# Kernel tuning notes

Measured on AMD Instinct MI355X. Metric: run time of the kernel, lower is better.

## Reference

```python
import jax, jax.numpy as jnp
import numpy as np

D_MODEL = 1024
NUM_HEADS = 16
HEAD_DIM = D_MODEL // NUM_HEADS
B, S, L_CACHE = 2, 1024, 1024


def setup_inputs() -> dict:
    key = jax.random.key(0)
    ks = jax.random.split(key, 12)
    sc = 1.0 / np.sqrt(D_MODEL)
    return {
        "x": jax.random.normal(ks[0], (B, S, D_MODEL), jnp.float32),
        "cache_k": jax.random.normal(ks[1], (B, NUM_HEADS, L_CACHE, HEAD_DIM), jnp.float32),
        "cache_v": jax.random.normal(ks[2], (B, NUM_HEADS, L_CACHE, HEAD_DIM), jnp.float32),
        "Wq": jax.random.normal(ks[3], (D_MODEL, D_MODEL), jnp.float32) * sc,
        "bq": jax.random.normal(ks[4], (D_MODEL,), jnp.float32) * 0.01,
        "Wk": jax.random.normal(ks[5], (D_MODEL, D_MODEL), jnp.float32) * sc,
        "bk": jax.random.normal(ks[6], (D_MODEL,), jnp.float32) * 0.01,
        "Wv": jax.random.normal(ks[7], (D_MODEL, D_MODEL), jnp.float32) * sc,
        "bv": jax.random.normal(ks[8], (D_MODEL,), jnp.float32) * 0.01,
        "Wo": jax.random.normal(ks[9], (D_MODEL, D_MODEL), jnp.float32) * sc,
        "bo": jax.random.normal(ks[10], (D_MODEL,), jnp.float32) * 0.01,
    }


def reference(x, cache_k, cache_v, Wq, bq, Wk, bk, Wv, bv, Wo, bo):
    b, s, d = x.shape
    h, hd = NUM_HEADS, HEAD_DIM
    # torch Linear: y = x @ W^T + b
    def proj(W, bias):
        y = jnp.einsum('bsd,ed->bse', x, W) + bias
        return y.reshape(b, s, h, hd).transpose(0, 2, 1, 3)  # [B,H,S,hd]
    Q = proj(Wq, bq)
    K = jnp.concatenate([cache_k, proj(Wk, bk)], axis=2)  # [B,H,T,hd]
    V = jnp.concatenate([cache_v, proj(Wv, bv)], axis=2)
    T = K.shape[2]
    scores = jnp.einsum('bhqd,bhkd->bhqk', Q, K) / jnp.sqrt(jnp.float32(hd))
    # causal mask with cache offset: query i sees keys j <= i + (T - s)
    offset = T - s
    q_idx = jnp.arange(s)[:, None]
    k_idx = jnp.arange(T)[None, :]
    mask = k_idx > (q_idx + offset)  # [S,T], True = masked
    scores = jnp.where(mask[None, None], -jnp.inf, scores)
    attn = jax.nn.softmax(scores, axis=-1)
    out = jnp.einsum('bhqk,bhkd->bhqd', attn, V)
    out = out.transpose(0, 2, 1, 3).reshape(b, s, d)
    return jnp.einsum('bsd,ed->bse', out, Wo) + bo
```

## Files before the change

kernel.cpp:

```cpp
#include <hip/hip_runtime.h>
#include <hip/hip_bf16.h>
#include <stdint.h>

typedef __bf16 bf16;
typedef __bf16 bf16x4 __attribute__((ext_vector_type(4)));
typedef __bf16 bf16x8 __attribute__((ext_vector_type(8)));
typedef float  f32x4  __attribute__((ext_vector_type(4)));

#define DEV __device__ __forceinline__

#define BB 2
#define HH 16
#define SS 1024
#define DD 1024
#define HD 64
#define LC 1024
#define TT 2048
#define OFFS 1024

DEV f32x4 mfma16(bf16x8 a, bf16x8 b, f32x4 c) {
    return __builtin_amdgcn_mfma_f32_16x16x32_bf16(a, b, c, 0, 0, 0);
}

DEV void async_load16(const bf16* g, bf16* lds) {
    auto gp = reinterpret_cast<const __attribute__((address_space(1))) void*>(
        reinterpret_cast<uintptr_t>(g));
    auto lp = reinterpret_cast<__attribute__((address_space(3))) void*>(
        reinterpret_cast<uintptr_t>(lds));
    __builtin_amdgcn_global_load_lds(gp, lp, 16, 0, 0);
}

__global__ __launch_bounds__(256) void cvt_all(
    const float* __restrict__ x,  bf16* __restrict__ xb,
    const float* __restrict__ w0, const float* __restrict__ w1,
    const float* __restrict__ w2, const float* __restrict__ w3,
    bf16* __restrict__ d0, bf16* __restrict__ d1,
    bf16* __restrict__ d2, bf16* __restrict__ d3,
    const float* __restrict__ ck, bf16* __restrict__ Kf,
    const float* __restrict__ cv, bf16* __restrict__ Vt) {
    __shared__ float tile[64][65];
    const int bid = blockIdx.x;
    const int tid = threadIdx.x;
    if (bid < 8192) {
        const float* s;
        bf16* d;
        int i;
        if (bid < 2048) {
            s = x; d = xb; i = bid * 256 + tid;
        } else if (bid < 6144) {
            int which = (bid - 2048) >> 10;
            s = which == 0 ? w0 : which == 1 ? w1 : which == 2 ? w2 : w3;
            d = which == 0 ? d0 : which == 1 ? d1 : which == 2 ? d2 : d3;
            i = ((bid - 2048) & 1023) * 256 + tid;
        } else {
            int ii = (bid - 6144) * 256 + tid;
            int bh  = ii >> 14;
            int rem = ii & 16383;
            float4 v = ((const float4*)ck)[ii];
            bf16x4 o;
            o[0] = (bf16)v.x; o[1] = (bf16)v.y; o[2] = (bf16)v.z; o[3] = (bf16)v.w;
            ((bf16x4*)(Kf + (size_t)bh * TT * HD))[rem] = o;
            return;
        }
        float4 v = ((const float4*)s)[i];
        bf16x4 o;
        o[0] = (bf16)v.x; o[1] = (bf16)v.y; o[2] = (bf16)v.z; o[3] = (bf16)v.w;
        ((bf16x4*)d)[i] = o;
    } else {
        int rem = bid - 8192;
        int bh = rem >> 4;
        int t0 = (rem & 15) * 64;
        int c4 = (tid & 15) * 4;
        int rr = tid >> 4;
        const float* src = cv + ((size_t)bh * LC + t0) * HD;
#pragma unroll
        for (int p = 0; p < 4; ++p) {
            int t = rr + p * 16;
            float4 v = *(const float4*)(src + (size_t)t * HD + c4);
            tile[c4 + 0][t] = v.x; tile[c4 + 1][t] = v.y;
            tile[c4 + 2][t] = v.z; tile[c4 + 3][t] = v.w;
        }
        __syncthreads();
        bf16* dst = Vt + (size_t)bh * HD * TT + t0;
#pragma unroll
        for (int p = 0; p < 4; ++p) {
            int d = rr + p * 16;
            int tc = (tid & 15) * 4;
            bf16x4 o;
            o[0] = (bf16)tile[d][tc + 0]; o[1] = (bf16)tile[d][tc + 1];
            o[2] = (bf16)tile[d][tc + 2]; o[3] = (bf16)tile[d][tc + 3];
            *(bf16x4*)(dst + (size_t)d * TT + tc) = o;
        }
    }
}

__global__ __launch_bounds__(256) void gemm_nt(
    const bf16* __restrict__ A, const bf16* __restrict__ W,
    const float* __restrict__ bq, const float* __restrict__ bk,
    const float* __restrict__ bv, const float* __restrict__ bo,
    bf16* __restrict__ Qb, bf16* __restrict__ Kf, bf16* __restrict__ Vt,
    float* __restrict__ Out, int is_oproj) {
    const int tid  = threadIdx.x;
    const int wv   = tid >> 6;
    const int lane = tid & 63;
    const int l16  = lane & 15;
    const int quad = lane >> 4;
    const int m0 = blockIdx.y * 64;
    const int n0 = blockIdx.x * 128;
    const int mode = is_oproj ? 3 : (n0 >> 10);
    const float* bias = (mode == 0) ? bq : (mode == 1) ? bk : (mode == 2) ? bv : bo;

    __shared__ __align__(16) bf16 As[2][64 * 64];
    __shared__ __align__(16) bf16 Bs[2][128 * 64];

    f32x4 acc[4][2];
#pragma unroll
    for (int i = 0; i < 4; ++i)
#pragma unroll
        for (int j = 0; j < 2; ++j) {
            f32x4 z = {0.f, 0.f, 0.f, 0.f};
            acc[i][j] = z;
        }

    auto stage = [&](int k0, int b) {
#pragma unroll
        for (int k = 0; k < 2; ++k) {
            int seg = k * 256 + tid;
            int row = seg >> 3;
            int c   = (seg & 7) ^ (row & 7);
            async_load16(A + (size_t)(m0 + row) * 1024 + k0 + c * 8, &As[b][seg * 8]);
        }
#pragma unroll
        for (int k = 0; k < 4; ++k) {
            int seg = k * 256 + tid;
            int row = seg >> 3;
            int c   = (seg & 7) ^ (row & 7);
            async_load16(W + (size_t)(n0 + row) * 1024 + k0 + c * 8, &Bs[b][seg * 8]);
        }
    };

    stage(0, 0);

    for (int it = 0; it < 16; ++it) {
        __syncthreads();
        const bf16* Ab = &As[it & 1][0];
        const bf16* Bb = &Bs[it & 1][0];
        if (it + 1 < 16) stage((it + 1) * 64, (it + 1) & 1);

#pragma unroll
        for (int kk = 0; kk < 2; ++kk) {
            bf16x8 af[4], bfr[2];
#pragma unroll
            for (int i = 0; i < 4; ++i) {
                int row = i * 16 + l16;
                int slot = (kk * 4 + quad) ^ (row & 7);
                af[i] = *(const bf16x8*)(Ab + (row * 8 + slot) * 8);
            }
#pragma unroll
            for (int j = 0; j < 2; ++j) {
                int row = wv * 32 + j * 16 + l16;
                int slot = (kk * 4 + quad) ^ (row & 7);
                bfr[j] = *(const bf16x8*)(Bb + (row * 8 + slot) * 8);
            }
#pragma unroll
            for (int i = 0; i < 4; ++i)
#pragma unroll
                for (int j = 0; j < 2; ++j)
                    acc[i][j] = mfma16(af[i], bfr[j], acc[i][j]);
        }
    }

#pragma unroll
    for (int i = 0; i < 4; ++i) {
#pragma unroll
        for (int j = 0; j < 2; ++j) {
            int n = n0 + wv * 32 + j * 16 + l16;
            float bval = bias[n & 1023];
#pragma unroll
            for (int r = 0; r < 4; ++r) {
                int m = m0 + i * 16 + quad * 4 + r;
                float v = acc[i][j][r] + bval;
                if (mode == 3) {
                    Out[(size_t)m * 1024 + n] = v;
                } else {
                    int b = m >> 10, s = m & 1023;
                    int h = (n & 1023) >> 6, d = n & 63;
                    int bh = b * HH + h;
                    if (mode == 0)
                        Qb[((size_t)bh * SS + s) * HD + d] = (bf16)v;
                    else if (mode == 1)
                        Kf[((size_t)bh * TT + LC + s) * HD + d] = (bf16)v;
                    else
                        Vt[((size_t)bh * HD + d) * TT + LC + s] = (bf16)v;
                }
            }
        }
    }
}

__global__ __launch_bounds__(256) void attn(const bf16* __restrict__ Qb,
                                            const bf16* __restrict__ Kf,
                                            const bf16* __restrict__ Vt,
                                            bf16* __restrict__ Ob) {
    const int i = blockIdx.x;
    const int bh = i & 31;
    const int qblk = (i < 256) ? (15 - (i >> 5)) : ((i >> 5) - 8);
    const int tid  = threadIdx.x;
    const int wv   = tid >> 6;
    const int lane = tid & 63;
    const int l16  = lane & 15;
    const int quad = lane >> 4;
    const int qb   = qblk * 64;
    const int qw   = qb + wv * 16;

    const bf16* Qp = Qb + ((size_t)bh * SS + qw) * HD;
    const bf16* Kp = Kf + (size_t)bh * TT * HD;
    const bf16* Vp = Vt + (size_t)bh * HD * TT;

    __shared__ __align__(16) bf16 Ks[2][64 * 64];
    __shared__ __align__(16) bf16 Vs[2][64 * 64];

    bf16x8 qf0 = *(const bf16x8*)(Qp + l16 * HD + quad * 8);
    bf16x8 qf1 = *(const bf16x8*)(Qp + l16 * HD + 32 + quad * 8);

    float lsum = 0.f;
    f32x4 o[4];
#pragma unroll
    for (int dt = 0; dt < 4; ++dt) {
        f32x4 z = {0.f, 0.f, 0.f, 0.f};
        o[dt] = z;
    }

    const int niters = qblk + 17;

    auto stage = [&](int tile, int b) {
        const int t0 = tile * 64;
#pragma unroll
        for (int j = 0; j < 2; ++j) {
            int seg = (j * 4 + wv) * 64 + lane;
            int row = seg >> 3;
            int gc  = (seg & 7) ^ (row & 7);
            async_load16(Kp + (size_t)(t0 + row) * HD + gc * 8, &Ks[b][seg * 8]);
            async_load16(Vp + (size_t)row * TT + t0 + gc * 8, &Vs[b][seg * 8]);
        }
    };

    stage(0, 0);

    const float C1 = 0.18033688f;
    const float C2 = -11.5415603f;

    for (int it = 0; it < niters; ++it) {
        __syncthreads();
        const bf16* Kb = &Ks[it & 1][0];
        const bf16* Vb = &Vs[it & 1][0];
        if (it + 1 < niters) stage(it + 1, (it + 1) & 1);

        const int t0 = it * 64;
        const bool full = (t0 + 63 <= qw + OFFS);

        f32x4 s[4];
#pragma unroll
        for (int kt = 0; kt < 4; ++kt) {
            int row = kt * 16 + l16;
            int swz = row & 7;
            bf16x8 ka = *(const bf16x8*)(Kb + (row * 8 + (quad ^ swz)) * 8);
            bf16x8 kb = *(const bf16x8*)(Kb + (row * 8 + ((4 + quad) ^ swz)) * 8);
            f32x4 z = {0.f, 0.f, 0.f, 0.f};
            z = mfma16(ka, qf0, z);
            z = mfma16(kb, qf1, z);
            s[kt] = z;
        }

        f32x4 p[4];
        if (full) {
#pragma unroll
            for (int kt = 0; kt < 4; ++kt)
#pragma unroll
                for (int r = 0; r < 4; ++r)
                    p[kt][r] = __builtin_amdgcn_exp2f(fmaf(s[kt][r], C1, C2));
        } else {
            const int qlim = qw + l16 + OFFS - t0;
#pragma unroll
            for (int kt = 0; kt < 4; ++kt)
#pragma unroll
                for (int r = 0; r < 4; ++r) {
                    int tl = kt * 16 + quad * 4 + r;
                    float e = __builtin_amdgcn_exp2f(fmaf(s[kt][r], C1, C2));
                    p[kt][r] = (tl <= qlim) ? e : 0.f;
                }
        }
#pragma unroll
        for (int kt = 0; kt < 4; ++kt)
            lsum += (p[kt][0] + p[kt][1]) + (p[kt][2] + p[kt][3]);

        bf16x8 pf0, pf1;
#pragma unroll
        for (int j = 0; j < 4; ++j) {
            pf0[j]     = (bf16)p[0][j];
            pf0[4 + j] = (bf16)p[1][j];
            pf1[j]     = (bf16)p[2][j];
            pf1[4 + j] = (bf16)p[3][j];
        }

        const int q1 = quad >> 1;
        const int h4 = (quad & 1) * 4;
#pragma unroll
        for (int dt = 0; dt < 4; ++dt) {
            int row = dt * 16 + l16;
            int swz = row & 7;
            bf16x4 v0 = *(const bf16x4*)(Vb + (row * 8 + ((0 + q1) ^ swz)) * 8 + h4);
            bf16x4 v1 = *(const bf16x4*)(Vb + (row * 8 + ((2 + q1) ^ swz)) * 8 + h4);
            bf16x4 v2 = *(const bf16x4*)(Vb + (row * 8 + ((4 + q1) ^ swz)) * 8 + h4);
            bf16x4 v3 = *(const bf16x4*)(Vb + (row * 8 + ((6 + q1) ^ swz)) * 8 + h4);
            bf16x8 vf0, vf1;
#pragma unroll
            for (int j = 0; j < 4; ++j) {
                vf0[j] = v0[j]; vf0[4 + j] = v1[j];
                vf1[j] = v2[j]; vf1[4 + j] = v3[j];
            }
            o[dt] = mfma16(vf0, pf0, o[dt]);
            o[dt] = mfma16(vf1, pf1, o[dt]);
        }
    }

    lsum += __shfl_xor(lsum, 16, 64);
    lsum += __shfl_xor(lsum, 32, 64);
    const float rl = 1.f / lsum;

    const int b = bh >> 4, h = bh & 15;
    const int q = qw + l16;
    bf16* op = Ob + (((size_t)(b * SS + q) * HH) + h) * HD;
#pragma unroll
    for (int dt = 0; dt < 4; ++dt) {
        bf16x4 w;
#pragma unroll
        for (int r = 0; r < 4; ++r) w[r] = (bf16)(o[dt][r] * rl);
        *(bf16x4*)(op + dt * 16 + quad * 4) = w;
    }
}

extern "C" void kernel_launch(void* const* d_in, const int* in_sizes, int n_in,
                              void* d_out, int out_size, void* d_ws, size_t ws_size,
                              hipStream_t stream) {
    const float* x   = (const float*)d_in[0];
    const float* ck  = (const float*)d_in[1];
    const float* cv  = (const float*)d_in[2];
    const float* Wq  = (const float*)d_in[3];
    const float* bq  = (const float*)d_in[4];
    const float* Wk  = (const float*)d_in[5];
    const float* bk  = (const float*)d_in[6];
    const float* Wv  = (const float*)d_in[7];
    const float* bv  = (const float*)d_in[8];
    const float* Wo  = (const float*)d_in[9];
    const float* bo  = (const float*)d_in[10];
    float* out = (float*)d_out;

    char* ws = (char*)d_ws;
    bf16* xb  = (bf16*)(ws);
    bf16* wqb = (bf16*)(ws + ( 4u << 20));
    bf16* wkb = (bf16*)(ws + ( 6u << 20));
    bf16* wvb = (bf16*)(ws + ( 8u << 20));
    bf16* wob = (bf16*)(ws + (10u << 20));
    bf16* Qb  = (bf16*)(ws + (12u << 20));
    bf16* Kf  = (bf16*)(ws + (16u << 20));
    bf16* Vt  = (bf16*)(ws + (24u << 20));
    bf16* Ob  = (bf16*)(ws + (32u << 20));

    cvt_all<<<8704, 256, 0, stream>>>(x, xb, Wq, Wk, Wv, Wo, wqb, wkb, wvb, wob,
                                      ck, Kf, cv, Vt);

    gemm_nt<<<dim3(24, 32), 256, 0, stream>>>(xb, wqb, bq, bk, bv, bo,
                                              Qb, Kf, Vt, out, 0);
    attn<<<512, 256, 0, stream>>>(Qb, Kf, Vt, Ob);
    gemm_nt<<<dim3(8, 32), 256, 0, stream>>>(Ob, wob, bq, bk, bv, bo,
                                             Qb, Kf, Vt, out, 1);
}
```

Baseline: 160.3 us.

## Split attention waves across query and key halves with LDS reduction

Each wave in the attention kernel now covers 32 queries and half of each 64-key tile, instead of 16 queries and the full tile. Each K fragment read from LDS feeds two query sub-tiles and each V fragment feeds two MFMAs, which cuts LDS read traffic per MFMA. Waves whose key half is fully masked skip the tile. The cost is an extra LDS reduction and barrier at the end to merge the two key-half partial outputs and row sums, plus more accumulator registers per wave.

```diff
diff --git a/kernel.cpp b/kernel.cpp
--- a/kernel.cpp
+++ b/kernel.cpp
@@ -207,11 +207,13 @@
     const int qblk = (i < 256) ? (15 - (i >> 5)) : ((i >> 5) - 8);
     const int tid  = threadIdx.x;
     const int wv   = tid >> 6;
+    const int qh   = wv & 1;
+    const int kh   = wv >> 1;
     const int lane = tid & 63;
     const int l16  = lane & 15;
     const int quad = lane >> 4;
     const int qb   = qblk * 64;
-    const int qw   = qb + wv * 16;
+    const int qw   = qb + qh * 32;
 
     const bf16* Qp = Qb + ((size_t)bh * SS + qw) * HD;
     const bf16* Kp = Kf + (size_t)bh * TT * HD;
@@ -220,16 +222,22 @@
     __shared__ __align__(16) bf16 Ks[2][64 * 64];
     __shared__ __align__(16) bf16 Vs[2][64 * 64];
 
-    bf16x8 qf0 = *(const bf16x8*)(Qp + l16 * HD + quad * 8);
-    bf16x8 qf1 = *(const bf16x8*)(Qp + l16 * HD + 32 + quad * 8);
-
-    float lsum = 0.f;
-    f32x4 o[4];
-#pragma unroll
-    for (int dt = 0; dt < 4; ++dt) {
-        f32x4 z = {0.f, 0.f, 0.f, 0.f};
-        o[dt] = z;
-    }
+    bf16x8 qf[2][2];
+#pragma unroll
+    for (int qs = 0; qs < 2; ++qs)
+#pragma unroll
+        for (int dc = 0; dc < 2; ++dc)
+            qf[qs][dc] = *(const bf16x8*)(Qp + (qs * 16 + l16) * HD + dc * 32 + quad * 8);
+
+    float lsum[2] = {0.f, 0.f};
+    f32x4 o[4][2];
+#pragma unroll
+    for (int dt = 0; dt < 4; ++dt)
+#pragma unroll
+        for (int qs = 0; qs < 2; ++qs) {
+            f32x4 z = {0.f, 0.f, 0.f, 0.f};
+            o[dt][qs] = z;
+        }
 
     const int niters = qblk + 17;
 
@@ -257,51 +265,63 @@
         if (it + 1 < niters) stage(it + 1, (it + 1) & 1);
 
         const int t0 = it * 64;
-        const bool full = (t0 + 63 <= qw + OFFS);
-
-        f32x4 s[4];
-#pragma unroll
-        for (int kt = 0; kt < 4; ++kt) {
-            int row = kt * 16 + l16;
+        const int kbase = kh * 32;
+        if (t0 + kbase > qw + 31 + OFFS) continue;
+        const bool full = (t0 + kbase + 31 <= qw + OFFS);
+
+        f32x4 s[2][2];
+#pragma unroll
+        for (int kt = 0; kt < 2; ++kt) {
+            int row = kbase + kt * 16 + l16;
             int swz = row & 7;
             bf16x8 ka = *(const bf16x8*)(Kb + (row * 8 + (quad ^ swz)) * 8);
             bf16x8 kb = *(const bf16x8*)(Kb + (row * 8 + ((4 + quad) ^ swz)) * 8);
-            f32x4 z = {0.f, 0.f, 0.f, 0.f};
-            z = mfma16(ka, qf0, z);
-            z = mfma16(kb, qf1, z);
-            s[kt] = z;
-        }
-
-        f32x4 p[4];
+#pragma unroll
+            for (int qs = 0; qs < 2; ++qs) {
+                f32x4 z = {0.f, 0.f, 0.f, 0.f};
+                z = mfma16(ka, qf[qs][0], z);
+                z = mfma16(kb, qf[qs][1], z);
+                s[kt][qs] = z;
+            }
+        }
+
+        f32x4 p[2][2];
         if (full) {
 #pragma unroll
-            for (int kt = 0; kt < 4; ++kt)
-#pragma unroll
-                for (int r = 0; r < 4; ++r)
-                    p[kt][r] = __builtin_amdgcn_exp2f(fmaf(s[kt][r], C1, C2));
+            for (int kt = 0; kt < 2; ++kt)
+#pragma unroll
+                for (int qs = 0; qs < 2; ++qs)
+#pragma unroll
+                    for (int r = 0; r < 4; ++r)
+                        p[kt][qs][r] = __builtin_amdgcn_exp2f(fmaf(s[kt][qs][r], C1, C2));
         } else {
-            const int qlim = qw + l16 + OFFS - t0;
-#pragma unroll
-            for (int kt = 0; kt < 4; ++kt)
-#pragma unroll
-                for (int r = 0; r < 4; ++r) {
-                    int tl = kt * 16 + quad * 4 + r;
-                    float e = __builtin_amdgcn_exp2f(fmaf(s[kt][r], C1, C2));
-                    p[kt][r] = (tl <= qlim) ? e : 0.f;
-                }
-        }
-#pragma unroll
-        for (int kt = 0; kt < 4; ++kt)
-            lsum += (p[kt][0] + p[kt][1]) + (p[kt][2] + p[kt][3]);
-
-        bf16x8 pf0, pf1;
-#pragma unroll
-        for (int j = 0; j < 4; ++j) {
-            pf0[j]     = (bf16)p[0][j];
-            pf0[4 + j] = (bf16)p[1][j];
-            pf1[j]     = (bf16)p[2][j];
-            pf1[4 + j] = (bf16)p[3][j];
-        }
+#pragma unroll
+            for (int qs = 0; qs < 2; ++qs) {
+                const int qlim = qw + qs * 16 + l16 + OFFS - t0;
+#pragma unroll
+                for (int kt = 0; kt < 2; ++kt)
+#pragma unroll
+                    for (int r = 0; r < 4; ++r) {
+                        int tl = kbase + kt * 16 + quad * 4 + r;
+                        float e = __builtin_amdgcn_exp2f(fmaf(s[kt][qs][r], C1, C2));
+                        p[kt][qs][r] = (tl <= qlim) ? e : 0.f;
+                    }
+            }
+        }
+#pragma unroll
+        for (int qs = 0; qs < 2; ++qs)
+#pragma unroll
+            for (int kt = 0; kt < 2; ++kt)
+                lsum[qs] += (p[kt][qs][0] + p[kt][qs][1]) + (p[kt][qs][2] + p[kt][qs][3]);
+
+        bf16x8 pf[2];
+#pragma unroll
+        for (int qs = 0; qs < 2; ++qs)
+#pragma unroll
+            for (int j = 0; j < 4; ++j) {
+                pf[qs][j]     = (bf16)p[0][qs][j];
+                pf[qs][4 + j] = (bf16)p[1][qs][j];
+            }
 
         const int q1 = quad >> 1;
         const int h4 = (quad & 1) * 4;
@@ -309,34 +329,67 @@
         for (int dt = 0; dt < 4; ++dt) {
             int row = dt * 16 + l16;
             int swz = row & 7;
-            bf16x4 v0 = *(const bf16x4*)(Vb + (row * 8 + ((0 + q1) ^ swz)) * 8 + h4);
-            bf16x4 v1 = *(const bf16x4*)(Vb + (row * 8 + ((2 + q1) ^ swz)) * 8 + h4);
-            bf16x4 v2 = *(const bf16x4*)(Vb + (row * 8 + ((4 + q1) ^ swz)) * 8 + h4);
-            bf16x4 v3 = *(const bf16x4*)(Vb + (row * 8 + ((6 + q1) ^ swz)) * 8 + h4);
-            bf16x8 vf0, vf1;
+            bf16x4 v0 = *(const bf16x4*)(Vb + (row * 8 + ((kh * 4 + q1) ^ swz)) * 8 + h4);
+            bf16x4 v1 = *(const bf16x4*)(Vb + (row * 8 + ((kh * 4 + 2 + q1) ^ swz)) * 8 + h4);
+            bf16x8 vf;
 #pragma unroll
             for (int j = 0; j < 4; ++j) {
-                vf0[j] = v0[j]; vf0[4 + j] = v1[j];
-                vf1[j] = v2[j]; vf1[4 + j] = v3[j];
-            }
-            o[dt] = mfma16(vf0, pf0, o[dt]);
-            o[dt] = mfma16(vf1, pf1, o[dt]);
-        }
-    }
-
-    lsum += __shfl_xor(lsum, 16, 64);
-    lsum += __shfl_xor(lsum, 32, 64);
-    const float rl = 1.f / lsum;
+                vf[j] = v0[j]; vf[4 + j] = v1[j];
+            }
+#pragma unroll
+            for (int qs = 0; qs < 2; ++qs)
+                o[dt][qs] = mfma16(vf, pf[qs], o[dt][qs]);
+        }
+    }
+
+#pragma unroll
+    for (int qs = 0; qs < 2; ++qs) {
+        lsum[qs] += __shfl_xor(lsum[qs], 16, 64);
+        lsum[qs] += __shfl_xor(lsum[qs], 32, 64);
+    }
+
+    __syncthreads();
+    float* So = (float*)&Ks[0][0];
+    float* Sl = (float*)&Vs[0][0];
+    if (kh == 1) {
+#pragma unroll
+        for (int dt = 0; dt < 4; ++dt)
+#pragma unroll
+            for (int qs = 0; qs < 2; ++qs)
+#pragma unroll
+                for (int r = 0; r < 4; ++r)
+                    So[(dt * 8 + qs * 4 + r) * 128 + qh * 64 + lane] = o[dt][qs][r];
+#pragma unroll
+        for (int qs = 0; qs < 2; ++qs)
+            Sl[qs * 128 + qh * 64 + lane] = lsum[qs];
+    }
+    __syncthreads();
+    if (kh == 1) return;
+
+#pragma unroll
+    for (int dt = 0; dt < 4; ++dt)
+#pragma unroll
+        for (int qs = 0; qs < 2; ++qs)
+#pragma unroll
+            for (int r = 0; r < 4; ++r)
+                o[dt][qs][r] += So[(dt * 8 + qs * 4 + r) * 128 + qh * 64 + lane];
+    float rl[2];
+#pragma unroll
+    for (int qs = 0; qs < 2; ++qs)
+        rl[qs] = 1.f / (lsum[qs] + Sl[qs * 128 + qh * 64 + lane]);
 
     const int b = bh >> 4, h = bh & 15;
-    const int q = qw + l16;
-    bf16* op = Ob + (((size_t)(b * SS + q) * HH) + h) * HD;
-#pragma unroll
-    for (int dt = 0; dt < 4; ++dt) {
-        bf16x4 w;
-#pragma unroll
-        for (int r = 0; r < 4; ++r) w[r] = (bf16)(o[dt][r] * rl);
-        *(bf16x4*)(op + dt * 16 + quad * 4) = w;
+#pragma unroll
+    for (int qs = 0; qs < 2; ++qs) {
+        const int q = qw + qs * 16 + l16;
+        bf16* op = Ob + (((size_t)(b * SS + q) * HH) + h) * HD;
+#pragma unroll
+        for (int dt = 0; dt < 4; ++dt) {
+            bf16x4 w;
+#pragma unroll
+            for (int r = 0; r < 4; ++r) w[r] = (bf16)(o[dt][qs][r] * rl[qs]);
+            *(bf16x4*)(op + dt * 16 + quad * 4) = w;
+        }
     }
 }
 
```

Result: no change. 162.5 us (+1.4%).
